# Optimization experiments

Hardware: AMD Instinct MI355X
Metric: run time of the kernel (lower is better)

Reference implementation:

```python
import jax, jax.numpy as jnp
import numpy as np
import math

HAD_BLOCK = 1024


def fwht(x):
    """Fast Walsh-Hadamard transform along the last axis (size must be power of 2)."""
    orig_shape = x.shape
    n = orig_shape[-1]
    x = x.reshape(-1, n)
    h = 1
    while h < n:  # log2(n) stages; static Python loop, jit-friendly
        x = x.reshape(-1, n // (2 * h), 2, h)
        a = x[:, :, 0, :]
        b = x[:, :, 1, :]
        x = jnp.stack([a + b, a - b], axis=2).reshape(-1, n)
        h *= 2
    return x.reshape(orig_shape)


def setup_inputs() -> dict:
    key = jax.random.key(0)
    kx, kw = jax.random.split(key)
    B, S, D_in, D_out = 4, 4096, 4096, 4096
    x = jax.random.normal(kx, (B, S, D_in), dtype=jnp.float32)
    # nn.Parameter(weight / sqrt(had_block_size)) in __init__
    weight = jax.random.normal(kw, (D_out, D_in), dtype=jnp.float32) / math.sqrt(HAD_BLOCK)
    return {"x": x, "weight": weight}


def reference(x, weight):
    n = x.shape[-1]
    padded = ((n - 1) // HAD_BLOCK + 1) * HAD_BLOCK
    if padded != n:
        pad_width = [(0, 0)] * (x.ndim - 1) + [(0, padded - n)]
        x = jnp.pad(x, pad_width)
    mult = padded // HAD_BLOCK
    xb = x.reshape(x.shape[:-1] + (mult, HAD_BLOCK))
    xb = fwht(xb) * (1.0 / math.sqrt(HAD_BLOCK))
    xh = xb.reshape(x.shape[:-1] + (mult * HAD_BLOCK,))
    # F.linear: x @ weight.T
    return jnp.einsum('bsi,oi->bso', xh, weight)
```

## Files before the change

### kernel.cpp

```cpp
#include <hip/hip_runtime.h>
#include <hip/hip_bf16.h>
#include <stdint.h>


typedef __attribute__((ext_vector_type(8))) short    short8;
typedef __attribute__((ext_vector_type(4))) float    f32x4;
typedef __attribute__((ext_vector_type(8))) uint16_t u16x8;

static constexpr int MDIM = 16384;
static constexpr int NDIM = 4096;
static constexpr int KDIM = 4096;
static constexpr int BM = 256, BN = 256, BK = 64;
static constexpr int NT = KDIM / BK;

__device__ __forceinline__ uint16_t f2bf(float f) {
  union { float f; uint32_t u; } c; c.f = f;
  uint32_t u = c.u;
  return (uint16_t)((u + 0x7FFFu + ((u >> 16) & 1u)) >> 16);
}

__global__ __launch_bounds__(256) void cvt_x_kernel(const float* __restrict__ x,
                                                    uint16_t* __restrict__ xb, int n8) {
  int stride = gridDim.x * blockDim.x;
  for (int t = blockIdx.x * blockDim.x + threadIdx.x; t < n8; t += stride) {
    const float4* p = reinterpret_cast<const float4*>(x + (size_t)t * 8);
    float4 a = p[0], b = p[1];
    u16x8 o;
    o[0] = f2bf(a.x); o[1] = f2bf(a.y); o[2] = f2bf(a.z); o[3] = f2bf(a.w);
    o[4] = f2bf(b.x); o[5] = f2bf(b.y); o[6] = f2bf(b.z); o[7] = f2bf(b.w);
    *reinterpret_cast<u16x8*>(xb + (size_t)t * 8) = o;
  }
}

__global__ __launch_bounds__(256) void fwht_w_kernel(const float* __restrict__ W,
                                                     uint16_t* __restrict__ Wh) {
  __shared__ float s[1024];
  const int tid = threadIdx.x;
  const size_t base = (size_t)blockIdx.x * 1024;
  reinterpret_cast<float4*>(s)[tid] = reinterpret_cast<const float4*>(W + base)[tid];
  __syncthreads();
  for (int h = 1; h < 1024; h <<= 1) {
    #pragma unroll
    for (int pp = 0; pp < 2; ++pp) {
      int p = tid + pp * 256;
      int q = p & (h - 1);
      int i = ((p - q) << 1) | q;
      float a = s[i], b = s[i + h];
      s[i] = a + b;
      s[i + h] = a - b;
    }
    __syncthreads();
  }
  #pragma unroll
  for (int pp = 0; pp < 4; ++pp) {
    int i = tid + pp * 256;
    Wh[base + i] = f2bf(s[i] * 0.03125f);
  }
}


#define FENCE asm volatile("" ::: "memory")
#define SBAR  do { FENCE; __builtin_amdgcn_s_barrier(); \
                   __builtin_amdgcn_sched_barrier(0); } while (0)
#define LGKM0 do { asm volatile("s_waitcnt lgkmcnt(0)" ::: "memory"); \
                   __builtin_amdgcn_sched_barrier(0); } while (0)
#define VMC(n) do { asm volatile("s_waitcnt vmcnt(" #n ")" ::: "memory"); \
                    __builtin_amdgcn_sched_barrier(0); } while (0)

#define LDA4(DST, BUF, MLO, KOFF)                                              \
  do { _Pragma("unroll")                                                       \
    for (int m_ = 0; m_ < 4; ++m_)                                             \
      DST[m_] = *(const short8*)(aRd + (BUF)*32768 + ((MLO)+m_)*2048 + (KOFF)); \
  } while (0)

#define LDB4(DST, BUF, KOFF)                                                   \
  do { _Pragma("unroll")                                                       \
    for (int n_ = 0; n_ < 4; ++n_)                                             \
      DST[n_] = *(const short8*)(bRd + (BUF)*32768 + n_*2048 + (KOFF));        \
  } while (0)

#define MF16(AF, BF, MB)                                                       \
  do { __builtin_amdgcn_s_setprio(1);                                          \
    _Pragma("unroll")                                                          \
    for (int m_ = 0; m_ < 4; ++m_)                                             \
      _Pragma("unroll")                                                        \
      for (int n_ = 0; n_ < 4; ++n_)                                           \
        acc[(MB)+m_][n_] = __builtin_amdgcn_mfma_f32_16x16x32_bf16(            \
            AF[m_], BF[n_], acc[(MB)+m_][n_], 0, 0, 0);                        \
    __builtin_amdgcn_s_setprio(0);                                             \
  } while (0)

#define ITER(T1, T2, T3, FIN)                                                  \
  do {                                                                         \
    short8 aL[4], aH[4], bK[4];                                                \
     SBAR;                                                            \
    LDB4(bK, 0, k0off); LDA4(aL, 0, 0, k0off);                                 \
    stageA(1, 0, (T1));                                                        \
    LGKM0; MF16(aL, bK, 0);                                                    \
     SBAR;                                                            \
    LDA4(aH, 0, 4, k0off);                                                     \
    stageA(1, 1, (T1)); stageB(1, 1, (T1));                                    \
    LGKM0; MF16(aH, bK, 4);                                                    \
     SBAR;                                                            \
    LDB4(bK, 0, k1off); LDA4(aL, 0, 0, k1off);                                 \
    LGKM0; MF16(aL, bK, 0);                                                    \
     SBAR;                                                            \
    LDA4(aH, 0, 4, k1off);                                                     \
    if (!(FIN)) stageB(0, 0, (T2));                                            \
    LGKM0; MF16(aH, bK, 4);                                                    \
    if (FIN) { VMC(0); } else { VMC(2); }                                      \
     SBAR;                                                            \
    LDB4(bK, 1, k0off); LDA4(aL, 1, 0, k0off);                                 \
    if (!(FIN)) stageA(0, 0, (T2));                                            \
    LGKM0; MF16(aL, bK, 0);                                                    \
     SBAR;                                                            \
    LDA4(aH, 1, 4, k0off);                                                     \
    if (!(FIN)) { stageA(0, 1, (T2)); stageB(0, 1, (T2)); }                    \
    LGKM0; MF16(aH, bK, 4);                                                    \
     SBAR;                                                            \
    LDB4(bK, 1, k1off); LDA4(aL, 1, 0, k1off);                                 \
    LGKM0; MF16(aL, bK, 0);                                                    \
     SBAR;                                                            \
    LDA4(aH, 1, 4, k1off);                                                     \
    if (!(FIN)) stageB(1, 0, (T3));                                            \
    LGKM0; MF16(aH, bK, 4);                                                    \
    if (!(FIN)) { VMC(2); }                                                    \
  } while (0)

__global__ __launch_bounds__(512, 2) void gemm_bt(const uint16_t* __restrict__ A,
                                                  const uint16_t* __restrict__ B,
                                                  float* __restrict__ C) {
  __shared__ __align__(16) uint16_t Ab[2][BM * BK];
  __shared__ __align__(16) uint16_t Bb[2][BN * BK];

  const int tid = threadIdx.x;
  const int wv  = tid >> 6;
  const int l   = tid & 63;

  const int wg = ((blockIdx.x & 7) << 7) | (blockIdx.x >> 3);
  const int tm = wg >> 4;
  const int tn = wg & 15;
  const int wm = wv >> 2;
  const int wn = wv & 3;

  const int t8  = tid >> 3;
  const int swz = (tid & 7) ^ ((tid >> 4) & 7);
  const uint16_t* sA = A + (size_t)(tm * BM + t8) * KDIM + swz * 8;
  const uint16_t* sB = B + (size_t)(tn * BN + t8) * KDIM + swz * 8;

  auto stageA = [&](int buf, int half, int tk) {
    #pragma unroll
    for (int j = 0; j < 2; ++j)
      __builtin_amdgcn_global_load_lds(
          (const __attribute__((address_space(1))) unsigned int*)
              (sA + (size_t)(half * 128 + j * 64) * KDIM + tk * BK),
          (__attribute__((address_space(3))) unsigned int*)
              ((char*)&Ab[buf][0] + half * 16384 + j * 8192 + wv * 1024),
          16, 0, 0);
  };
  auto stageB = [&](int buf, int half, int tk) {
    #pragma unroll
    for (int j = 0; j < 2; ++j)
      __builtin_amdgcn_global_load_lds(
          (const __attribute__((address_space(1))) unsigned int*)
              (sB + (size_t)(half * 128 + j * 64) * KDIM + tk * BK),
          (__attribute__((address_space(3))) unsigned int*)
              ((char*)&Bb[buf][0] + half * 16384 + j * 8192 + wv * 1024),
          16, 0, 0);
  };

  const int lA = l & 15, hi = l >> 4;
  const int xr = (lA >> 1) & 7;
  const int k0off = (hi ^ xr) * 16;
  const int k1off = k0off ^ 64;
  const char* aRd = (const char*)&Ab[0][0] + (wm * 128 + lA) * 128;
  const char* bRd = (const char*)&Bb[0][0] + (wn * 64 + lA) * 128;

  f32x4 acc[8][4] = {};

  stageA(0, 0, 0); stageA(0, 1, 0); stageB(0, 0, 0); stageB(0, 1, 0);
  stageB(1, 0, 1);
  VMC(2);

  #pragma unroll 1
  for (int i = 0; i < NT / 2 - 1; ++i)
    ITER(2 * i + 1, 2 * i + 2, 2 * i + 3, 0);
  ITER(NT - 1, 0, 0, 1);

  float* Cp = C + (size_t)(tm * BM + wm * 128) * NDIM + tn * BN + wn * 64;
  const int co = hi * 4;
  #pragma unroll
  for (int m = 0; m < 8; ++m)
    #pragma unroll
    for (int n = 0; n < 4; ++n)
      #pragma unroll
      for (int j = 0; j < 4; ++j)
        Cp[(size_t)(m * 16 + co + j) * NDIM + n * 16 + lA] = acc[m][n][j];
}

extern "C" void kernel_launch(void* const* d_in, const int* in_sizes, int n_in,
                              void* d_out, int out_size, void* d_ws, size_t ws_size,
                              hipStream_t stream) {
  (void)in_sizes; (void)n_in; (void)out_size; (void)ws_size;
  const float* x = (const float*)d_in[0];
  const float* w = (const float*)d_in[1];
  float* out = (float*)d_out;

  uint16_t* xb = (uint16_t*)d_ws;
  uint16_t* wh = xb + (size_t)MDIM * KDIM;

  cvt_x_kernel<<<2048, 256, 0, stream>>>(x, xb, (int)((MDIM * (size_t)KDIM) / 8));
  fwht_w_kernel<<<(NDIM * KDIM) / 1024, 256, 0, stream>>>(w, wh);
  gemm_bt<<<(MDIM / BM) * (NDIM / BN), 512, 0, stream>>>(xb, wh, out);
}
```

Before: 596.4 us.

## Software-pipeline LDS fragment loads one phase ahead of MFMA groups

Restructures the GEMM main loop so LDS reads for the next MFMA group are issued before the current group's MFMAs, using separate even/odd fragment register sets. The explicit lgkmcnt(0) waits are removed in favour of scheduling barriers, leaving the compiler to insert the needed waits so LDS latency overlaps matrix math. This raises VGPR pressure under the 512-thread, 2-block launch bound and risks spills or hazards around the shared buffer reuse.

```diff
diff --git a/kernel.cpp b/kernel.cpp
--- a/kernel.cpp
+++ b/kernel.cpp
@@ -62,8 +62,7 @@
 #define FENCE asm volatile("" ::: "memory")
 #define SBAR  do { FENCE; __builtin_amdgcn_s_barrier(); \
                    __builtin_amdgcn_sched_barrier(0); } while (0)
-#define LGKM0 do { asm volatile("s_waitcnt lgkmcnt(0)" ::: "memory"); \
-                   __builtin_amdgcn_sched_barrier(0); } while (0)
+#define SCHED0 __builtin_amdgcn_sched_barrier(0)
 #define VMC(n) do { asm volatile("s_waitcnt vmcnt(" #n ")" ::: "memory"); \
                     __builtin_amdgcn_sched_barrier(0); } while (0)
 
@@ -92,39 +91,42 @@
 
 #define ITER(T1, T2, T3, FIN)                                                  \
   do {                                                                         \
-    short8 aL[4], aH[4], bK[4];                                                \
-     SBAR;                                                            \
-    LDB4(bK, 0, k0off); LDA4(aL, 0, 0, k0off);                                 \
+     SBAR;                                                            \
     stageA(1, 0, (T1));                                                        \
-    LGKM0; MF16(aL, bK, 0);                                                    \
-     SBAR;                                                            \
-    LDA4(aH, 0, 4, k0off);                                                     \
+    LDA4(aHe, 0, 4, k0off);                                                    \
+    SCHED0; MF16(aLe, bKe, 0);                                                 \
+     SBAR;                                                            \
     stageA(1, 1, (T1)); stageB(1, 1, (T1));                                    \
-    LGKM0; MF16(aH, bK, 4);                                                    \
-     SBAR;                                                            \
-    LDB4(bK, 0, k1off); LDA4(aL, 0, 0, k1off);                                 \
-    LGKM0; MF16(aL, bK, 0);                                                    \
-     SBAR;                                                            \
-    LDA4(aH, 0, 4, k1off);                                                     \
+    LDB4(bKo, 0, k1off); LDA4(aLo, 0, 0, k1off);                               \
+    SCHED0; MF16(aHe, bKe, 4);                                                 \
+     SBAR;                                                            \
+    LDA4(aHo, 0, 4, k1off);                                                    \
+    SCHED0; MF16(aLo, bKo, 0);                                                 \
+     SBAR;                                                            \
     if (!(FIN)) stageB(0, 0, (T2));                                            \
-    LGKM0; MF16(aH, bK, 4);                                                    \
     if (FIN) { VMC(0); } else { VMC(2); }                                      \
-     SBAR;                                                            \
-    LDB4(bK, 1, k0off); LDA4(aL, 1, 0, k0off);                                 \
+    SBAR;                 \
+    LDB4(bKe, 1, k0off); LDA4(aLe, 1, 0, k0off);                               \
+    SCHED0; MF16(aHo, bKo, 4);                                                 \
+     SBAR;                                                            \
     if (!(FIN)) stageA(0, 0, (T2));                                            \
-    LGKM0; MF16(aL, bK, 0);                                                    \
-     SBAR;                                                            \
-    LDA4(aH, 1, 4, k0off);                                                     \
+    LDA4(aHe, 1, 4, k0off);                                                    \
+    SCHED0; MF16(aLe, bKe, 0);                                                 \
+     SBAR;                                                            \
     if (!(FIN)) { stageA(0, 1, (T2)); stageB(0, 1, (T2)); }                    \
-    LGKM0; MF16(aH, bK, 4);                                                    \
-     SBAR;                                                            \
-    LDB4(bK, 1, k1off); LDA4(aL, 1, 0, k1off);                                 \
-    LGKM0; MF16(aL, bK, 0);                                                    \
-     SBAR;                                                            \
-    LDA4(aH, 1, 4, k1off);                                                     \
-    if (!(FIN)) stageB(1, 0, (T3));                                            \
-    LGKM0; MF16(aH, bK, 4);                                                    \
-    if (!(FIN)) { VMC(2); }                                                    \
+    LDB4(bKo, 1, k1off); LDA4(aLo, 1, 0, k1off);                               \
+    SCHED0; MF16(aHe, bKe, 4);                                                 \
+     SBAR;                                                            \
+    LDA4(aHo, 1, 4, k1off);                                                    \
+    SCHED0; MF16(aLo, bKo, 0);                                                 \
+     SBAR;                                                            \
+    if (!(FIN)) {                                                              \
+      stageB(1, 0, (T3));                                                      \
+      VMC(2);                                                                  \
+      SBAR;               \
+      LDB4(bKe, 0, k0off); LDA4(aLe, 0, 0, k0off);                             \
+    }                                                                          \
+    SCHED0; MF16(aHo, bKo, 4);                                                 \
   } while (0)
 
 __global__ __launch_bounds__(512, 2) void gemm_bt(const uint16_t* __restrict__ A,
@@ -177,10 +179,13 @@
   const char* bRd = (const char*)&Bb[0][0] + (wn * 64 + lA) * 128;
 
   f32x4 acc[8][4] = {};
+  short8 aLe[4], aHe[4], bKe[4], aLo[4], aHo[4], bKo[4];
 
   stageA(0, 0, 0); stageA(0, 1, 0); stageB(0, 0, 0); stageB(0, 1, 0);
   stageB(1, 0, 1);
   VMC(2);
+  SBAR;
+  LDB4(bKe, 0, k0off); LDA4(aLe, 0, 0, k0off);
 
   #pragma unroll 1
   for (int i = 0; i < NT / 2 - 1; ++i)
```

Result: slower. 697.0 us (+16.9%).

## Restructure GEMM main loop into quadrant-based LDS reads with reordered staging

Applied to the files above, without the earlier changes.

Reorganizes each K-tile's MFMA work into four 4x2 quadrant sub-blocks that cover both K halves per LDS read, so A and B fragments are reused across quadrants instead of reloaded per K half. Global-to-LDS staging is redistributed across the quadrants, with one extra A stage issued ahead in the prologue and the vmcnt waits relaxed. The aim is to cut LDS read traffic and improve overlap of loads with MFMA. It raises register pressure (more live fragments) and reworks the barrier and waitcnt sequencing, which risks races or stalls.

```diff
diff --git a/kernel.cpp b/kernel.cpp
--- a/kernel.cpp
+++ b/kernel.cpp
@@ -64,67 +64,80 @@
                    __builtin_amdgcn_sched_barrier(0); } while (0)
 #define LGKM0 do { asm volatile("s_waitcnt lgkmcnt(0)" ::: "memory"); \
                    __builtin_amdgcn_sched_barrier(0); } while (0)
+#define LGKM8 do { asm volatile("s_waitcnt lgkmcnt(8)" ::: "memory"); \
+                   __builtin_amdgcn_sched_barrier(0); } while (0)
 #define VMC(n) do { asm volatile("s_waitcnt vmcnt(" #n ")" ::: "memory"); \
                     __builtin_amdgcn_sched_barrier(0); } while (0)
 
-#define LDA4(DST, BUF, MLO, KOFF)                                              \
+#define LDAQ(DST, BUF, MQ)                                                     \
   do { _Pragma("unroll")                                                       \
-    for (int m_ = 0; m_ < 4; ++m_)                                             \
-      DST[m_] = *(const short8*)(aRd + (BUF)*32768 + ((MLO)+m_)*2048 + (KOFF)); \
-  } while (0)
-
-#define LDB4(DST, BUF, KOFF)                                                   \
+    for (int k_ = 0; k_ < 2; ++k_)                                             \
+      _Pragma("unroll")                                                        \
+      for (int m_ = 0; m_ < 4; ++m_)                                           \
+        DST[k_ * 4 + m_] = *(const short8*)(aRd + (BUF)*32768 +                \
+            ((MQ)*64 + m_*16)*128 + (k_ ? k1off : k0off));                     \
+  } while (0)
+
+#define LDBQ(DST, BUF, NQ)                                                     \
   do { _Pragma("unroll")                                                       \
-    for (int n_ = 0; n_ < 4; ++n_)                                             \
-      DST[n_] = *(const short8*)(bRd + (BUF)*32768 + n_*2048 + (KOFF));        \
-  } while (0)
-
-#define MF16(AF, BF, MB)                                                       \
+    for (int k_ = 0; k_ < 2; ++k_)                                             \
+      _Pragma("unroll")                                                        \
+      for (int n_ = 0; n_ < 2; ++n_)                                           \
+        DST[k_ * 2 + n_] = *(const short8*)(bRd + (BUF)*32768 +                \
+            ((NQ)*32 + n_*16)*128 + (k_ ? k1off : k0off));                     \
+  } while (0)
+
+#define MFQ(AF, BF, MB, NB)                                                    \
   do { __builtin_amdgcn_s_setprio(1);                                          \
     _Pragma("unroll")                                                          \
-    for (int m_ = 0; m_ < 4; ++m_)                                             \
+    for (int k_ = 0; k_ < 2; ++k_)                                             \
       _Pragma("unroll")                                                        \
-      for (int n_ = 0; n_ < 4; ++n_)                                           \
-        acc[(MB)+m_][n_] = __builtin_amdgcn_mfma_f32_16x16x32_bf16(            \
-            AF[m_], BF[n_], acc[(MB)+m_][n_], 0, 0, 0);                        \
+      for (int m_ = 0; m_ < 4; ++m_)                                           \
+        _Pragma("unroll")                                                      \
+        for (int n_ = 0; n_ < 2; ++n_)                                         \
+          acc[(MB)+m_][(NB)+n_] = __builtin_amdgcn_mfma_f32_16x16x32_bf16(     \
+              AF[k_*4+m_], BF[k_*2+n_], acc[(MB)+m_][(NB)+n_], 0, 0, 0);       \
     __builtin_amdgcn_s_setprio(0);                                             \
   } while (0)
 
 #define ITER(T1, T2, T3, FIN)                                                  \
   do {                                                                         \
-    short8 aL[4], aH[4], bK[4];                                                \
-     SBAR;                                                            \
-    LDB4(bK, 0, k0off); LDA4(aL, 0, 0, k0off);                                 \
-    stageA(1, 0, (T1));                                                        \
-    LGKM0; MF16(aL, bK, 0);                                                    \
-     SBAR;                                                            \
-    LDA4(aH, 0, 4, k0off);                                                     \
-    stageA(1, 1, (T1)); stageB(1, 1, (T1));                                    \
-    LGKM0; MF16(aH, bK, 4);                                                    \
-     SBAR;                                                            \
-    LDB4(bK, 0, k1off); LDA4(aL, 0, 0, k1off);                                 \
-    LGKM0; MF16(aL, bK, 0);                                                    \
-     SBAR;                                                            \
-    LDA4(aH, 0, 4, k1off);                                                     \
+    short8 a0[8], a1[8], b0[4], b1[4];                                         \
+                                                   \
+    LDAQ(a0, 0, 0); LDBQ(b0, 0, 0);                                            \
+    stageA(1, 1, (T1));                                                        \
+    LGKM8;                                                                     \
+    SBAR; LGKM0; MFQ(a0, b0, 0, 0); SBAR;                                      \
+                                                   \
+    LDBQ(b1, 0, 1);                                                            \
+    stageB(1, 1, (T1));                                                        \
+    SBAR; LGKM0; MFQ(a0, b1, 0, 2); SBAR;                                      \
+                                                   \
+    LDAQ(a1, 0, 1);                                                            \
     if (!(FIN)) stageB(0, 0, (T2));                                            \
-    LGKM0; MF16(aH, bK, 4);                                                    \
-    if (FIN) { VMC(0); } else { VMC(2); }                                      \
-     SBAR;                                                            \
-    LDB4(bK, 1, k0off); LDA4(aL, 1, 0, k0off);                                 \
+    SBAR; LGKM0; MFQ(a1, b1, 4, 2); SBAR;                                      \
+                          \
     if (!(FIN)) stageA(0, 0, (T2));                                            \
-    LGKM0; MF16(aL, bK, 0);                                                    \
-     SBAR;                                                            \
-    LDA4(aH, 1, 4, k0off);                                                     \
-    if (!(FIN)) { stageA(0, 1, (T2)); stageB(0, 1, (T2)); }                    \
-    LGKM0; MF16(aH, bK, 4);                                                    \
-     SBAR;                                                            \
-    LDB4(bK, 1, k1off); LDA4(aL, 1, 0, k1off);                                 \
-    LGKM0; MF16(aL, bK, 0);                                                    \
-     SBAR;                                                            \
-    LDA4(aH, 1, 4, k1off);                                                     \
+    MFQ(a1, b0, 4, 0);                                                         \
+    if (FIN) { VMC(0); } else { VMC(4); }                                      \
+    SBAR;                                                                      \
+                                                             \
+    LDAQ(a0, 1, 0); LDBQ(b0, 1, 0);                                            \
+    if (!(FIN)) stageA(0, 1, (T2));                                            \
+    LGKM8;                                                                     \
+    SBAR; LGKM0; MFQ(a0, b0, 0, 0); SBAR;                                      \
+                                                             \
+    LDBQ(b1, 1, 1);                                                            \
+    if (!(FIN)) stageB(0, 1, (T2));                                            \
+    SBAR; LGKM0; MFQ(a0, b1, 0, 2); SBAR;                                      \
+                                                             \
+    LDAQ(a1, 1, 1);                                                            \
     if (!(FIN)) stageB(1, 0, (T3));                                            \
-    LGKM0; MF16(aH, bK, 4);                                                    \
-    if (!(FIN)) { VMC(2); }                                                    \
+    SBAR; LGKM0; MFQ(a1, b1, 4, 2); SBAR;                                      \
+                                                   \
+    if (!(FIN)) stageA(1, 0, (T3));                                            \
+    MFQ(a1, b0, 4, 0);                                                         \
+    if (!(FIN)) { VMC(4); SBAR; }                                              \
   } while (0)
 
 __global__ __launch_bounds__(512, 2) void gemm_bt(const uint16_t* __restrict__ A,
@@ -179,8 +192,9 @@
   f32x4 acc[8][4] = {};
 
   stageA(0, 0, 0); stageA(0, 1, 0); stageB(0, 0, 0); stageB(0, 1, 0);
-  stageB(1, 0, 1);
-  VMC(2);
+  stageB(1, 0, 1); stageA(1, 0, 1);
+  VMC(4);
+  SBAR;
 
   #pragma unroll 1
   for (int i = 0; i < NT / 2 - 1; ++i)
```

Result: slower. 613.3 us (+2.8%).
